# Optimization experiments

Measured on AMD Instinct MI355X. Metric: run time of the kernel, lower is better.

Reference implementation:

```python
import jax, jax.numpy as jnp
import numpy as np

# Graph dimensions (homogeneous node ordering per hetero2homo: [function, input, output])
N_F, N_I, N_O = 2000, 500, 500
N = N_F + N_I + N_O
C = 8                 # hidden channels per function node
H = N_F * C           # total hidden width
B = 256
E_FF, E_IF, E_FO = 40000, 5000, 2000
E = E_FF + E_IF + E_FO
EPS = 1e-5


def _build_graph():
    rng = np.random.default_rng(0)
    src_ff = rng.integers(0, N_F, E_FF)
    dst_ff = rng.integers(0, N_F, E_FF)
    src_if = rng.integers(N_F, N_F + N_I, E_IF)          # input -> function
    dst_if = rng.integers(0, N_F, E_IF)
    src_fo = rng.integers(0, N_F, E_FO)                   # function -> output
    dst_fo = rng.integers(N_F + N_I, N, E_FO)
    src = np.concatenate([src_ff, src_if, src_fo])
    dst = np.concatenate([dst_ff, dst_if, dst_fo])
    edge_index = jnp.asarray(np.stack([src, dst]), dtype=jnp.int32)
    mask = np.zeros(N, dtype=bool)
    mask[N_F + N_I:] = True
    return edge_index, jnp.asarray(mask)


def setup_inputs() -> dict:
    key = jax.random.key(0)
    k_x, k_w1, k_b1, k_w2, k_b2 = jax.random.split(key, 5)
    edge_index, output_node_mask = _build_graph()
    scale = 0.1  # xavier-ish for small fan-in/out
    return {
        "x": jax.random.normal(k_x, (B, N), dtype=jnp.float32),
        "w1": jax.random.normal(k_w1, (E, C), dtype=jnp.float32) * scale,
        "b1": jax.random.normal(k_b1, (H,), dtype=jnp.float32) * 0.01,
        "gamma": jnp.ones((H,), dtype=jnp.float32),
        "beta": jnp.zeros((H,), dtype=jnp.float32),
        "w2": jax.random.normal(k_w2, (E, C), dtype=jnp.float32) * scale,
        "b2": jax.random.normal(k_b2, (E,), dtype=jnp.float32) * 0.01,
        "edge_index": edge_index,
        "output_node_mask": output_node_mask,
        "layers": 10,
    }


def reference(x, w1, b1, gamma, beta, w2, b2, edge_index, output_node_mask, layers):
    src, dst = edge_index[0], edge_index[1]
    # W_in structure: hidden channel k of function node n receives edge e iff dst[e]==n.
    # Edges whose dst is not a function node are structurally absent -> route to dummy segment N_F.
    dst_seg = jnp.where(dst < N_F, dst, N_F)
    # W_out structure: edge e receives hidden channels of function node src[e]; zero otherwise.
    src_is_func = src < N_F
    src_clip = jnp.where(src_is_func, src, 0)

    xe = x[:, src]  # node2edge: (B, E)
    for _ in range(layers):
        # lin_in: sparse (E x H) matmul == per-edge outer product scatter-added onto dst node channels
        contrib = xe.T[:, :, None] * w1[:, None, :]                       # (E, B, C)
        hid = jax.ops.segment_sum(contrib, dst_seg, num_segments=N_F + 1)[:N_F]  # (N_F, B, C)
        h = hid.transpose(1, 0, 2).reshape(B, H) + b1                      # (B, H)
        # layer norm then nonlin (norm_first=True)
        mu = h.mean(-1, keepdims=True)
        var = h.var(-1, keepdims=True)
        h = (h - mu) * jax.lax.rsqrt(var + EPS) * gamma + beta
        h = jax.nn.elu(h)
        # lin_out: sparse (H x E) matmul == gather src-node channels, dot with per-edge weights
        hn = h.reshape(B, N_F, C)
        out_e = jnp.einsum('bec,ec->be', hn[:, src_clip, :], w2)
        out_e = jnp.where(src_is_func[None, :], out_e, 0.0) + b2[None, :]
        xe = xe + out_e                                                    # residual
    xe = xe / layers
    # edge2node: scatter-add edge features onto output nodes only
    xm = jnp.where(output_node_mask[dst][None, :], xe, 0.0)
    out = jax.ops.segment_sum(xm.T, dst, num_segments=output_node_mask.shape[0]).T  # (B, N)
    return out
```

## Files before the change

kernel.cpp:

```cpp
#include <hip/hip_runtime.h>
#include <cmath>
#include <cstdint>

#define N_F    2000
#define N_I    500
#define N_O    500
#define N_ALL  3000
#define C      8
#define H      16000
#define B      256
#define E_FF   40000
#define E_IF   5000
#define E_FO   2000
#define E_ALL  47000
#define LAYERS 10
#define EPSF   1e-5f
#define RED    32

static __device__ __forceinline__ unsigned short f2bf(float f) {
    unsigned int u = __float_as_uint(f);
    unsigned int r = (u + 0x7FFFu + ((u >> 16) & 1u)) >> 16;
    return (unsigned short)r;
}
static __device__ __forceinline__ float bf2f(unsigned short h) {
    return __uint_as_float(((unsigned int)h) << 16);
}


__global__ void k_zero_cnt(int* cntA, int* cntB, int* cntC, int* cntD) {
    int tid = threadIdx.x;
    for (int i = tid; i < N_F; i += 1024) { cntA[i] = 0; cntB[i] = 0; cntC[i] = 0; }
    for (int i = tid; i < N_O; i += 1024) cntD[i] = 0;
}

__global__ void k_count(const int* __restrict__ src, const int* __restrict__ dst,
                        int* cntA, int* cntB, int* cntC, int* cntD) {
    int e = blockIdx.x * 256 + threadIdx.x;
    if (e >= E_ALL) return;
    int s = src[e], d = dst[e];
    if (e < E_FF)             { atomicAdd(&cntA[d], 1); atomicAdd(&cntB[d], 1); atomicAdd(&cntC[s], 1); }
    else if (e < E_FF + E_IF) { atomicAdd(&cntA[d], 1); }
    else                      { atomicAdd(&cntD[d - (N_F + N_I)], 1); }
}

__global__ void k_scan(const int* cntA, const int* cntC, const int* cntD,
                       int* rsA, int* rsC, int* rsD,
                       int* curA, int* curC, int* curD) {
    const int* cnt; int* rs; int* cur; int len;
    if      (blockIdx.x == 0) { cnt = cntA; rs = rsA; cur = curA; len = N_F; }
    else if (blockIdx.x == 1) { cnt = cntC; rs = rsC; cur = curC; len = N_F; }
    else                      { cnt = cntD; rs = rsD; cur = curD; len = N_O; }
    __shared__ int buf[1024];
    __shared__ int carry;
    int tid = threadIdx.x;
    if (tid == 0) carry = 0;
    __syncthreads();
    for (int base0 = 0; base0 < len; base0 += 1024) {
        int i = base0 + tid;
        int v = (i < len) ? cnt[i] : 0;
        buf[tid] = v;
        __syncthreads();
        for (int off = 1; off < 1024; off <<= 1) {
            int t = (tid >= off) ? buf[tid - off] : 0;
            __syncthreads();
            buf[tid] += t;
            __syncthreads();
        }
        int excl = carry + buf[tid] - v;
        if (i < len) { rs[i] = excl; cur[i] = excl; }
        int tot = buf[1023];
        __syncthreads();
        if (tid == 0) carry += tot;
        __syncthreads();
    }
    if (tid == 0) rs[len] = carry;
}

__global__ void k_fill(const int* __restrict__ src, const int* __restrict__ dst,
                       int* curA, int* curC, int* curD,
                       int* eidA, int* eidC, int* eidD) {
    int e = blockIdx.x * 256 + threadIdx.x;
    if (e >= E_ALL) return;
    int s = src[e], d = dst[e];
    if (e < E_FF) {
        int a = atomicAdd(&curA[d], 1); eidA[a] = e;
        int p = atomicAdd(&curC[s], 1); eidC[p] = e;
    } else if (e < E_FF + E_IF) {
        int a = atomicAdd(&curA[d], 1); eidA[a] = e;
    } else {
        int k = atomicAdd(&curD[d - (N_F + N_I)], 1); eidD[k] = e;
    }
}

__global__ void k_wsort(const int* __restrict__ rsA, int* eidA,
                        const int* __restrict__ rsC, int* eidC,
                        const int* __restrict__ rsD, int* eidD) {
    int w = blockIdx.x * 4 + (threadIdx.x >> 6);
    int lane = threadIdx.x & 63;
    const int* rs; int* eid; int n;
    if      (w < 2000) { rs = rsA; eid = eidA; n = w; }
    else if (w < 4000) { rs = rsC; eid = eidC; n = w - 2000; }
    else if (w < 4500) { rs = rsD; eid = eidD; n = w - 4000; }
    else return;
    int beg = rs[n], end = rs[n + 1], len = end - beg;
    if (len <= 1) return;
    if (len <= 64) {
        int v = (lane < len) ? eid[beg + lane] : 0x7fffffff;
        int rank = 0;
        for (int j = 0; j < 64; ++j) {
            int o = __shfl(v, j, 64);
            rank += (o < v) ? 1 : 0;
        }
        if (lane < len) eid[beg + rank] = v;
    } else if (lane == 0) {
        for (int i = beg + 1; i < end; ++i) {
            int key = eid[i];
            int j = i - 1;
            while (j >= beg && eid[j] > key) { eid[j + 1] = eid[j]; --j; }
            eid[j + 1] = key;
        }
    }
}


__global__ void k_xT(const float* __restrict__ x, float* __restrict__ xT) {
    __shared__ float t[32][33];
    int tx = threadIdx.x, ty = threadIdx.y;
    int n = blockIdx.x * 32 + tx, b = blockIdx.y * 32 + ty;
    if (n < N_ALL) t[ty][tx] = x[b * N_ALL + n];
    __syncthreads();
    int n2 = blockIdx.x * 32 + ty, b2 = blockIdx.y * 32 + tx;
    if (n2 < N_ALL) xT[n2 * B + b2] = t[tx][ty];
}

__global__ void k_base(const float* __restrict__ xT, const float* __restrict__ w1,
                       const float* __restrict__ b1, const float* __restrict__ b2,
                       const int* __restrict__ rsA, const int* __restrict__ eidA,
                       const int* __restrict__ srcv,
                       float* __restrict__ baseG, float* __restrict__ bbG) {
    int n = blockIdx.x, tid = threadIdx.x;
    int beg = rsA[n], end = rsA[n + 1];
    float acc[C] = {0.f,0.f,0.f,0.f,0.f,0.f,0.f,0.f};
    float bba[C] = {0.f,0.f,0.f,0.f,0.f,0.f,0.f,0.f};
    const float4* w14 = (const float4*)w1;
    for (int a = beg; a < end; ++a) {
        int e = eidA[a];
        float xv = xT[srcv[e] * B + tid];
        float bv = b2[e];
        float4 u0 = w14[e * 2], u1 = w14[e * 2 + 1];
        acc[0] += u0.x * xv; acc[1] += u0.y * xv; acc[2] += u0.z * xv; acc[3] += u0.w * xv;
        acc[4] += u1.x * xv; acc[5] += u1.y * xv; acc[6] += u1.z * xv; acc[7] += u1.w * xv;
        bba[0] += u0.x * bv; bba[1] += u0.y * bv; bba[2] += u0.z * bv; bba[3] += u0.w * bv;
        bba[4] += u1.x * bv; bba[5] += u1.y * bv; bba[6] += u1.z * bv; bba[7] += u1.w * bv;
    }
    #pragma unroll
    for (int c = 0; c < C; ++c) baseG[(n * C + c) * B + tid] = acc[c] + b1[n * C + c];
    if (tid == 0) {
        #pragma unroll
        for (int c = 0; c < C; ++c) bbG[n * C + c] = bba[c];
    }
}


__global__ void f_hidstat(const float* __restrict__ baseG, const float* __restrict__ bbG,
                          const float* __restrict__ w1, const unsigned short* __restrict__ qbf,
                          const int* __restrict__ rsA, const int* __restrict__ eidA,
                          const int* __restrict__ cntB,
                          unsigned short* __restrict__ hidbf, float* __restrict__ bp, int t) {
    int n = blockIdx.x, tid = threadIdx.x;
    const float4* w14 = (const float4*)w1;
    float tf = (float)t;
    float hid[C];
    #pragma unroll
    for (int c = 0; c < C; ++c) hid[c] = baseG[(n * C + c) * B + tid] + tf * bbG[n * C + c];
    if (t > 0) {
        int beg = rsA[n], m = cntB[n];
        for (int j = beg; j < beg + m; ++j) {
            int e = eidA[j];
            float qv = bf2f(qbf[e * B + tid]);
            float4 u0 = w14[e * 2], u1 = w14[e * 2 + 1];
            hid[0] += u0.x * qv; hid[1] += u0.y * qv; hid[2] += u0.z * qv; hid[3] += u0.w * qv;
            hid[4] += u1.x * qv; hid[5] += u1.y * qv; hid[6] += u1.z * qv; hid[7] += u1.w * qv;
        }
    }
    float s1 = 0.f, s2 = 0.f;
    #pragma unroll
    for (int c = 0; c < C; ++c) {
        hidbf[(n * C + c) * B + tid] = f2bf(hid[c]);
        s1 += hid[c]; s2 += hid[c] * hid[c];
    }
    bp[(n * 2 + 0) * B + tid] = s1;
    bp[(n * 2 + 1) * B + tid] = s2;
}

__global__ void f_red(const float* __restrict__ bp, float* __restrict__ p2) {
    int blk = blockIdx.x, tid = threadIdx.x;
    float a1 = 0.f, a2 = 0.f;
    for (int i = blk; i < N_F; i += RED) {
        a1 += bp[(i * 2 + 0) * B + tid];
        a2 += bp[(i * 2 + 1) * B + tid];
    }
    p2[(blk * 2 + 0) * B + tid] = a1;
    p2[(blk * 2 + 1) * B + tid] = a2;
}

__global__ void f_upd(const unsigned short* __restrict__ hidbf, const float* __restrict__ p2,
                      const float* __restrict__ gamma, const float* __restrict__ beta,
                      const float* __restrict__ w2, const int* __restrict__ rsC,
                      const int* __restrict__ eidC,
                      float* __restrict__ Sg, unsigned short* __restrict__ qbf, int t) {
    int n = blockIdx.x, tid = threadIdx.x;
    const float4* w24 = (const float4*)w2;
    float S1 = 0.f, S2 = 0.f;
    #pragma unroll
    for (int k = 0; k < RED; ++k) {
        S1 += p2[(k * 2 + 0) * B + tid];
        S2 += p2[(k * 2 + 1) * B + tid];
    }
    float mu  = S1 * (1.0f / H);
    float var = S2 * (1.0f / H) - mu * mu;
    float rsq = rsqrtf(var + EPSF);
    float Sn[C];
    #pragma unroll
    for (int c = 0; c < C; ++c) {
        float v = bf2f(hidbf[(n * C + c) * B + tid]);
        v = (v - mu) * rsq * gamma[n * C + c] + beta[n * C + c];
        v = (v > 0.f) ? v : expm1f(v);
        Sn[c] = (t == 0) ? v : (Sg[(n * C + c) * B + tid] + v);
    }
    #pragma unroll
    for (int c = 0; c < C; ++c) Sg[(n * C + c) * B + tid] = Sn[c];
    if (t < LAYERS - 1) {
        int beg = rsC[n], end = rsC[n + 1];
        for (int p = beg; p < end; ++p) {
            int e = eidC[p];
            float4 u0 = w24[e * 2], u1 = w24[e * 2 + 1];
            float qv = u0.x * Sn[0] + u0.y * Sn[1] + u0.z * Sn[2] + u0.w * Sn[3]
                     + u1.x * Sn[4] + u1.y * Sn[5] + u1.z * Sn[6] + u1.w * Sn[7];
            qbf[e * B + tid] = f2bf(qv);
        }
    }
}


__global__ void f_zero_out(float* __restrict__ out) {
    int i = blockIdx.x * 256 + threadIdx.x;
    ((float4*)out)[i] = make_float4(0.f, 0.f, 0.f, 0.f);
}

__global__ void f_out(const float* __restrict__ xT, const float* __restrict__ Sg,
                      const int* __restrict__ rsD, const int* __restrict__ eidD,
                      const int* __restrict__ srcv, const float* __restrict__ w2,
                      const float* __restrict__ b2, float* __restrict__ out) {
    int o = blockIdx.x, tid = threadIdx.x;
    const float4* w24 = (const float4*)w2;
    float acc = 0.f;
    int beg = rsD[o], end = rsD[o + 1];
    for (int k = beg; k < end; ++k) {
        int e = eidD[k];
        int s = srcv[e];
        float4 u0 = w24[e * 2], u1 = w24[e * 2 + 1];
        float dot = u0.x * Sg[(s * C + 0) * B + tid] + u0.y * Sg[(s * C + 1) * B + tid]
                  + u0.z * Sg[(s * C + 2) * B + tid] + u0.w * Sg[(s * C + 3) * B + tid]
                  + u1.x * Sg[(s * C + 4) * B + tid] + u1.y * Sg[(s * C + 5) * B + tid]
                  + u1.z * Sg[(s * C + 6) * B + tid] + u1.w * Sg[(s * C + 7) * B + tid];
        acc += xT[s * B + tid] + dot + (float)LAYERS * b2[e];
    }
    out[tid * N_ALL + (N_F + N_I + o)] = acc * (1.0f / LAYERS);
}


static inline char* alignup(char* p) { return (char*)(((uintptr_t)p + 255) & ~(uintptr_t)255); }

extern "C" void kernel_launch(void* const* d_in, const int* in_sizes, int n_in,
                              void* d_out, int out_size, void* d_ws, size_t ws_size,
                              hipStream_t stream) {
    const float* x     = (const float*)d_in[0];
    const float* w1    = (const float*)d_in[1];
    const float* b1    = (const float*)d_in[2];
    const float* gamma = (const float*)d_in[3];
    const float* beta  = (const float*)d_in[4];
    const float* w2    = (const float*)d_in[5];
    const float* b2    = (const float*)d_in[6];
    const int*   ei    = (const int*)d_in[7];
    const int* srcv = ei;
    const int* dstv = ei + E_ALL;
    float* out = (float*)d_out;

    char* p = (char*)d_ws;
    unsigned short* qbf   = (unsigned short*)p; p += (size_t)E_FF * B * 2; p = alignup(p);
    unsigned short* hidbf = (unsigned short*)p; p += (size_t)H * B * 2;    p = alignup(p);
    float* Sg    = (float*)p; p += (size_t)H * B * 4;        p = alignup(p);
    float* baseG = (float*)p; p += (size_t)H * B * 4;        p = alignup(p);
    float* xT    = (float*)p; p += (size_t)N_ALL * B * 4;    p = alignup(p);
    float* bp    = (float*)p; p += (size_t)N_F * 2 * B * 4;  p = alignup(p);
    float* p2    = (float*)p; p += (size_t)RED * 2 * B * 4;  p = alignup(p);
    float* bbG   = (float*)p; p += (size_t)N_F * C * 4;      p = alignup(p);
    int* cntA = (int*)p; p += N_F * 4;        p = alignup(p);
    int* cntB = (int*)p; p += N_F * 4;        p = alignup(p);
    int* cntC = (int*)p; p += N_F * 4;        p = alignup(p);
    int* cntD = (int*)p; p += N_O * 4;        p = alignup(p);
    int* curA = (int*)p; p += N_F * 4;        p = alignup(p);
    int* curC = (int*)p; p += N_F * 4;        p = alignup(p);
    int* curD = (int*)p; p += N_O * 4;        p = alignup(p);
    int* rsA  = (int*)p; p += (N_F + 1) * 4;  p = alignup(p);
    int* rsC  = (int*)p; p += (N_F + 1) * 4;  p = alignup(p);
    int* rsD  = (int*)p; p += (N_O + 1) * 4;  p = alignup(p);
    int* eidA = (int*)p; p += (size_t)(E_FF + E_IF) * 4; p = alignup(p);
    int* eidC = (int*)p; p += (size_t)E_FF * 4; p = alignup(p);
    int* eidD = (int*)p; p += (size_t)E_FO * 4; p = alignup(p);

    hipLaunchKernelGGL(k_zero_cnt, dim3(1), dim3(1024), 0, stream, cntA, cntB, cntC, cntD);
    hipLaunchKernelGGL(k_count, dim3((E_ALL + 255) / 256), dim3(256), 0, stream,
                       srcv, dstv, cntA, cntB, cntC, cntD);
    hipLaunchKernelGGL(k_scan, dim3(3), dim3(1024), 0, stream,
                       cntA, cntC, cntD, rsA, rsC, rsD, curA, curC, curD);
    hipLaunchKernelGGL(k_fill, dim3((E_ALL + 255) / 256), dim3(256), 0, stream,
                       srcv, dstv, curA, curC, curD, eidA, eidC, eidD);
    hipLaunchKernelGGL(k_wsort, dim3(1125), dim3(256), 0, stream,
                       rsA, eidA, rsC, eidC, rsD, eidD);
    hipLaunchKernelGGL(k_xT, dim3((N_ALL + 31) / 32, B / 32), dim3(32, 32), 0, stream, x, xT);
    hipLaunchKernelGGL(k_base, dim3(N_F), dim3(256), 0, stream,
                       xT, w1, b1, b2, rsA, eidA, srcv, baseG, bbG);

    hipLaunchKernelGGL(f_zero_out, dim3(750), dim3(256), 0, stream, out);
    for (int t = 0; t < LAYERS; ++t) {
        hipLaunchKernelGGL(f_hidstat, dim3(N_F), dim3(256), 0, stream,
                           baseG, bbG, w1, qbf, rsA, eidA, cntB, hidbf, bp, t);
        hipLaunchKernelGGL(f_red, dim3(RED), dim3(256), 0, stream, bp, p2);
        hipLaunchKernelGGL(f_upd, dim3(N_F), dim3(256), 0, stream,
                           hidbf, p2, gamma, beta, w2, rsC, eidC, Sg, qbf, t);
    }
    hipLaunchKernelGGL(f_out, dim3(N_O), dim3(256), 0, stream,
                       xT, Sg, rsD, eidD, srcv, w2, b2, out);
}
```

Baseline: 742.3 us.

## Reorder edge buffers by destination and fold reduction into hidstat via last-block atomics

Permutes the per-edge q buffer and w1/w2 weights so that f_hidstat reads contiguous rows in destination-sorted order, with no indirection through eidA. f_upd then scatters into the permuted slots. The separate f_red launch is removed: the last RED blocks of f_hidstat spin on an atomic counter and perform the cross-block statistic reduction. This cuts the layer launches from three to two and improves read locality. The cost is a few extra setup kernels and a spin-wait that relies on all blocks being able to make progress.

```diff
diff --git a/kernel.cpp b/kernel.cpp
--- a/kernel.cpp
+++ b/kernel.cpp
@@ -27,10 +27,11 @@
 }
 
 
-__global__ void k_zero_cnt(int* cntA, int* cntB, int* cntC, int* cntD) {
+__global__ void k_zero_cnt(int* cntA, int* cntB, int* cntC, int* cntD, int* cnt_red) {
     int tid = threadIdx.x;
     for (int i = tid; i < N_F; i += 1024) { cntA[i] = 0; cntB[i] = 0; cntC[i] = 0; }
     for (int i = tid; i < N_O; i += 1024) cntD[i] = 0;
+    if (tid < LAYERS) cnt_red[tid] = 0;
 }
 
 __global__ void k_count(const int* __restrict__ src, const int* __restrict__ dst,
@@ -43,13 +44,14 @@
     else                      { atomicAdd(&cntD[d - (N_F + N_I)], 1); }
 }
 
-__global__ void k_scan(const int* cntA, const int* cntC, const int* cntD,
-                       int* rsA, int* rsC, int* rsD,
-                       int* curA, int* curC, int* curD) {
+__global__ void k_scan(const int* cntA, const int* cntB, const int* cntC, const int* cntD,
+                       int* rsA, int* rsB2, int* rsC, int* rsD,
+                       int* curA, int* curB, int* curC, int* curD) {
     const int* cnt; int* rs; int* cur; int len;
-    if      (blockIdx.x == 0) { cnt = cntA; rs = rsA; cur = curA; len = N_F; }
-    else if (blockIdx.x == 1) { cnt = cntC; rs = rsC; cur = curC; len = N_F; }
-    else                      { cnt = cntD; rs = rsD; cur = curD; len = N_O; }
+    if      (blockIdx.x == 0) { cnt = cntA; rs = rsA;  cur = curA; len = N_F; }
+    else if (blockIdx.x == 1) { cnt = cntB; rs = rsB2; cur = curB; len = N_F; }
+    else if (blockIdx.x == 2) { cnt = cntC; rs = rsC;  cur = curC; len = N_F; }
+    else                      { cnt = cntD; rs = rsD;  cur = curD; len = N_O; }
     __shared__ int buf[1024];
     __shared__ int carry;
     int tid = threadIdx.x;
@@ -120,6 +122,31 @@
             eid[j + 1] = key;
         }
     }
+}
+
+__global__ void k_posB(const int* __restrict__ rsA, const int* __restrict__ eidA,
+                       const int* __restrict__ cntB, const int* __restrict__ rsB2,
+                       const float* __restrict__ w1, int* posB, float* jw1) {
+    int n = blockIdx.x * 256 + threadIdx.x;
+    if (n >= N_F) return;
+    int a0 = rsA[n], j0 = rsB2[n], m = cntB[n];
+    for (int k = 0; k < m; ++k) {
+        int e = eidA[a0 + k];
+        int j = j0 + k;
+        posB[e] = j;
+        #pragma unroll
+        for (int c = 0; c < C; ++c) jw1[j * C + c] = w1[e * C + c];
+    }
+}
+
+__global__ void k_posC(const int* __restrict__ eidC, const int* __restrict__ posB,
+                       const float* __restrict__ w2, int* jposC, float* w2C) {
+    int p = blockIdx.x * 256 + threadIdx.x;
+    if (p >= E_FF) return;
+    int e = eidC[p];
+    jposC[p] = posB[e];
+    #pragma unroll
+    for (int c = 0; c < C; ++c) w2C[p * C + c] = w2[e * C + c];
 }
 
 
@@ -162,23 +189,23 @@
 }
 
 
-__global__ void f_hidstat(const float* __restrict__ baseG, const float* __restrict__ bbG,
-                          const float* __restrict__ w1, const unsigned short* __restrict__ qbf,
-                          const int* __restrict__ rsA, const int* __restrict__ eidA,
-                          const int* __restrict__ cntB,
-                          unsigned short* __restrict__ hidbf, float* __restrict__ bp, int t) {
+__global__ __launch_bounds__(256) void f_hidstat(
+    const float* __restrict__ baseG, const float* __restrict__ bbG,
+    const float* __restrict__ jw1, const unsigned short* __restrict__ qbf,
+    const int* __restrict__ rsB2,
+    unsigned short* __restrict__ hidbf, float* __restrict__ bp,
+    float* __restrict__ p2, int* __restrict__ cnt_red, int t) {
     int n = blockIdx.x, tid = threadIdx.x;
-    const float4* w14 = (const float4*)w1;
+    const float4* jw14 = (const float4*)jw1;
     float tf = (float)t;
     float hid[C];
     #pragma unroll
     for (int c = 0; c < C; ++c) hid[c] = baseG[(n * C + c) * B + tid] + tf * bbG[n * C + c];
     if (t > 0) {
-        int beg = rsA[n], m = cntB[n];
-        for (int j = beg; j < beg + m; ++j) {
-            int e = eidA[j];
-            float qv = bf2f(qbf[e * B + tid]);
-            float4 u0 = w14[e * 2], u1 = w14[e * 2 + 1];
+        int beg = rsB2[n], end = rsB2[n + 1];
+        for (int j = beg; j < end; ++j) {
+            float qv = bf2f(qbf[j * B + tid]);
+            float4 u0 = jw14[j * 2], u1 = jw14[j * 2 + 1];
             hid[0] += u0.x * qv; hid[1] += u0.y * qv; hid[2] += u0.z * qv; hid[3] += u0.w * qv;
             hid[4] += u1.x * qv; hid[5] += u1.y * qv; hid[6] += u1.z * qv; hid[7] += u1.w * qv;
         }
@@ -191,26 +218,35 @@
     }
     bp[(n * 2 + 0) * B + tid] = s1;
     bp[(n * 2 + 1) * B + tid] = s2;
-}
-
-__global__ void f_red(const float* __restrict__ bp, float* __restrict__ p2) {
-    int blk = blockIdx.x, tid = threadIdx.x;
-    float a1 = 0.f, a2 = 0.f;
-    for (int i = blk; i < N_F; i += RED) {
-        a1 += bp[(i * 2 + 0) * B + tid];
-        a2 += bp[(i * 2 + 1) * B + tid];
-    }
-    p2[(blk * 2 + 0) * B + tid] = a1;
-    p2[(blk * 2 + 1) * B + tid] = a2;
-}
-
-__global__ void f_upd(const unsigned short* __restrict__ hidbf, const float* __restrict__ p2,
-                      const float* __restrict__ gamma, const float* __restrict__ beta,
-                      const float* __restrict__ w2, const int* __restrict__ rsC,
-                      const int* __restrict__ eidC,
-                      float* __restrict__ Sg, unsigned short* __restrict__ qbf, int t) {
+
+    __threadfence();
+    __syncthreads();
+    __shared__ int s_old;
+    if (tid == 0) s_old = atomicAdd(&cnt_red[t], 1);
+    __syncthreads();
+    int old = s_old;
+    if (old >= N_F - RED) {
+        while (__hip_atomic_load(&cnt_red[t], __ATOMIC_ACQUIRE, __HIP_MEMORY_SCOPE_AGENT) < N_F)
+            __builtin_amdgcn_s_sleep(2);
+        int slice = old - (N_F - RED);
+        float a1 = 0.f, a2 = 0.f;
+        for (int i = slice; i < N_F; i += RED) {
+            a1 += bp[(i * 2 + 0) * B + tid];
+            a2 += bp[(i * 2 + 1) * B + tid];
+        }
+        p2[(slice * 2 + 0) * B + tid] = a1;
+        p2[(slice * 2 + 1) * B + tid] = a2;
+    }
+}
+
+__global__ __launch_bounds__(256) void f_upd(
+    const unsigned short* __restrict__ hidbf, const float* __restrict__ p2,
+    const float* __restrict__ gamma, const float* __restrict__ beta,
+    const float* __restrict__ w2C, const int* __restrict__ jposC,
+    const int* __restrict__ rsC,
+    float* __restrict__ Sg, unsigned short* __restrict__ qbf, int t) {
     int n = blockIdx.x, tid = threadIdx.x;
-    const float4* w24 = (const float4*)w2;
+    const float4* w24 = (const float4*)w2C;
     float S1 = 0.f, S2 = 0.f;
     #pragma unroll
     for (int k = 0; k < RED; ++k) {
@@ -233,11 +269,11 @@
     if (t < LAYERS - 1) {
         int beg = rsC[n], end = rsC[n + 1];
         for (int p = beg; p < end; ++p) {
-            int e = eidC[p];
-            float4 u0 = w24[e * 2], u1 = w24[e * 2 + 1];
+            int j = jposC[p];
+            float4 u0 = w24[p * 2], u1 = w24[p * 2 + 1];
             float qv = u0.x * Sn[0] + u0.y * Sn[1] + u0.z * Sn[2] + u0.w * Sn[3]
                      + u1.x * Sn[4] + u1.y * Sn[5] + u1.z * Sn[6] + u1.w * Sn[7];
-            qbf[e * B + tid] = f2bf(qv);
+            qbf[j * B + tid] = f2bf(qv);
         }
     }
 }
@@ -296,29 +332,40 @@
     float* bp    = (float*)p; p += (size_t)N_F * 2 * B * 4;  p = alignup(p);
     float* p2    = (float*)p; p += (size_t)RED * 2 * B * 4;  p = alignup(p);
     float* bbG   = (float*)p; p += (size_t)N_F * C * 4;      p = alignup(p);
+    float* jw1   = (float*)p; p += (size_t)E_FF * C * 4;     p = alignup(p);
+    float* w2C   = (float*)p; p += (size_t)E_FF * C * 4;     p = alignup(p);
+    int* posB  = (int*)p; p += (size_t)E_FF * 4;  p = alignup(p);
+    int* jposC = (int*)p; p += (size_t)E_FF * 4;  p = alignup(p);
+    int* cnt_red = (int*)p; p += LAYERS * 4;      p = alignup(p);
     int* cntA = (int*)p; p += N_F * 4;        p = alignup(p);
     int* cntB = (int*)p; p += N_F * 4;        p = alignup(p);
     int* cntC = (int*)p; p += N_F * 4;        p = alignup(p);
     int* cntD = (int*)p; p += N_O * 4;        p = alignup(p);
     int* curA = (int*)p; p += N_F * 4;        p = alignup(p);
+    int* curB = (int*)p; p += N_F * 4;        p = alignup(p);
     int* curC = (int*)p; p += N_F * 4;        p = alignup(p);
     int* curD = (int*)p; p += N_O * 4;        p = alignup(p);
     int* rsA  = (int*)p; p += (N_F + 1) * 4;  p = alignup(p);
+    int* rsB2 = (int*)p; p += (N_F + 1) * 4;  p = alignup(p);
     int* rsC  = (int*)p; p += (N_F + 1) * 4;  p = alignup(p);
     int* rsD  = (int*)p; p += (N_O + 1) * 4;  p = alignup(p);
     int* eidA = (int*)p; p += (size_t)(E_FF + E_IF) * 4; p = alignup(p);
     int* eidC = (int*)p; p += (size_t)E_FF * 4; p = alignup(p);
     int* eidD = (int*)p; p += (size_t)E_FO * 4; p = alignup(p);
 
-    hipLaunchKernelGGL(k_zero_cnt, dim3(1), dim3(1024), 0, stream, cntA, cntB, cntC, cntD);
+    hipLaunchKernelGGL(k_zero_cnt, dim3(1), dim3(1024), 0, stream, cntA, cntB, cntC, cntD, cnt_red);
     hipLaunchKernelGGL(k_count, dim3((E_ALL + 255) / 256), dim3(256), 0, stream,
                        srcv, dstv, cntA, cntB, cntC, cntD);
-    hipLaunchKernelGGL(k_scan, dim3(3), dim3(1024), 0, stream,
-                       cntA, cntC, cntD, rsA, rsC, rsD, curA, curC, curD);
+    hipLaunchKernelGGL(k_scan, dim3(4), dim3(1024), 0, stream,
+                       cntA, cntB, cntC, cntD, rsA, rsB2, rsC, rsD, curA, curB, curC, curD);
     hipLaunchKernelGGL(k_fill, dim3((E_ALL + 255) / 256), dim3(256), 0, stream,
                        srcv, dstv, curA, curC, curD, eidA, eidC, eidD);
     hipLaunchKernelGGL(k_wsort, dim3(1125), dim3(256), 0, stream,
                        rsA, eidA, rsC, eidC, rsD, eidD);
+    hipLaunchKernelGGL(k_posB, dim3((N_F + 255) / 256), dim3(256), 0, stream,
+                       rsA, eidA, cntB, rsB2, w1, posB, jw1);
+    hipLaunchKernelGGL(k_posC, dim3((E_FF + 255) / 256), dim3(256), 0, stream,
+                       eidC, posB, w2, jposC, w2C);
     hipLaunchKernelGGL(k_xT, dim3((N_ALL + 31) / 32, B / 32), dim3(32, 32), 0, stream, x, xT);
     hipLaunchKernelGGL(k_base, dim3(N_F), dim3(256), 0, stream,
                        xT, w1, b1, b2, rsA, eidA, srcv, baseG, bbG);
@@ -326,10 +373,9 @@
     hipLaunchKernelGGL(f_zero_out, dim3(750), dim3(256), 0, stream, out);
     for (int t = 0; t < LAYERS; ++t) {
         hipLaunchKernelGGL(f_hidstat, dim3(N_F), dim3(256), 0, stream,
-                           baseG, bbG, w1, qbf, rsA, eidA, cntB, hidbf, bp, t);
-        hipLaunchKernelGGL(f_red, dim3(RED), dim3(256), 0, stream, bp, p2);
+                           baseG, bbG, jw1, qbf, rsB2, hidbf, bp, p2, cnt_red, t);
         hipLaunchKernelGGL(f_upd, dim3(N_F), dim3(256), 0, stream,
-                           hidbf, p2, gamma, beta, w2, rsC, eidC, Sg, qbf, t);
+                           hidbf, p2, gamma, beta, w2C, jposC, rsC, Sg, qbf, t);
     }
     hipLaunchKernelGGL(f_out, dim3(N_O), dim3(256), 0, stream,
                        xT, Sg, rsD, eidD, srcv, w2, b2, out);
```

New measurement: 2.723 ms. +266.9%, slower.
